# Performance work log

Hardware: AMD Instinct MI355X
Metric: run time of the kernel (lower is better)

## Reference

```python
import jax, jax.numpy as jnp
import numpy as np
from jax import lax

H, W = 32, 32
HEADS = 8
EPS_LN = 1e-5


def layer_norm(x, g, b):
    mu = jnp.mean(x, axis=-1, keepdims=True)
    var = jnp.mean((x - mu) ** 2, axis=-1, keepdims=True)
    return (x - mu) * lax.rsqrt(var + EPS_LN) * g + b


def l2norm(x):  # F.normalize along last dim, eps=1e-12
    n = jnp.sqrt(jnp.sum(x * x, axis=-1, keepdims=True))
    return x / jnp.maximum(n, 1e-12)


def channel_attention(x, qkv_w, temp, proj_w, proj_b):
    B, N, C = x.shape
    d = C // HEADS
    qkv = (x @ qkv_w).reshape(B, N, 3, HEADS, d).transpose(2, 0, 3, 1, 4)  # [3,B,h,N,d]
    q, k, v = qkv[0], qkv[1], qkv[2]
    q = l2norm(q.swapaxes(-2, -1))  # [B,h,d,N], normalized over N
    k = l2norm(k.swapaxes(-2, -1))
    v = v.swapaxes(-2, -1)          # [B,h,d,N]
    attn = jnp.einsum('bhdn,bhen->bhde', q, k) * temp  # [B,h,d,d]
    attn = jax.nn.softmax(attn, axis=-1)
    out = jnp.einsum('bhde,bhen->bhdn', attn, v)       # [B,h,d,N]
    out = out.transpose(0, 3, 1, 2).reshape(B, N, C)
    return out @ proj_w + proj_b


def cross_attention(x1, x2, rp_w, rp_b, cn_g, cn_b):
    # head_count = 1 (efficient/linear attention)
    B, N, D = x1.shape
    keys = x2.swapaxes(1, 2)            # [B,D,N]
    values = x1.swapaxes(1, 2)          # [B,D,N]
    key = jax.nn.softmax(keys, axis=2)  # softmax over tokens
    query = jax.nn.softmax(keys, axis=1)  # softmax over channels
    context = jnp.einsum('bdn,ben->bde', key, values)     # [B,Dk,Dv]
    attended = jnp.einsum('bde,bdn->ben', context, query)  # [B,Dv,N]
    agg = attended.reshape(B, D, H, W)
    # 1x1 conv reprojection D -> 2D
    rep = jnp.einsum('bdhw,ed->behw', agg, rp_w) + rp_b[None, :, None, None]
    rep = rep.reshape(B, 2 * D, N).transpose(0, 2, 1)     # [B,N,2D]
    return layer_norm(rep, cn_g, cn_b)


def mix_ffn(x, fc1_w, fc1_b, dw_w, dw_b, fc2_w, fc2_b):
    B, N, _ = x.shape
    c2 = fc1_w.shape[1]
    h1 = x @ fc1_w + fc1_b                                 # [B,N,c2]
    t = h1.swapaxes(1, 2).reshape(B, c2, H, W)
    conv = lax.conv_general_dilated(
        t, dw_w, window_strides=(1, 1), padding='SAME',
        feature_group_count=c2,
        dimension_numbers=('NCHW', 'OIHW', 'NCHW')) + dw_b[None, :, None, None]
    h2 = conv.reshape(B, c2, N).swapaxes(1, 2)             # [B,N,c2]
    return jax.nn.gelu(h2, approximate=False) @ fc2_w + fc2_b


def reference(x1, x2, ln1_g, ln1_b, ca_qkv_w, ca_temp, ca_proj_w, ca_proj_b,
              ln3_g, ln3_b, rp_w, rp_b, cn_g, cn_b, ln2_g, ln2_b,
              fc1_w, fc1_b, dw_w, dw_b, fc2_w, fc2_b):
    # NOTE: original code uses norm1 + channel_attn1 on BOTH streams
    channel1 = x1 + channel_attention(layer_norm(x1, ln1_g, ln1_b), ca_qkv_w, ca_temp, ca_proj_w, ca_proj_b)
    channel2 = x2 + channel_attention(layer_norm(x2, ln1_g, ln1_b), ca_qkv_w, ca_temp, ca_proj_w, ca_proj_b)
    n1 = layer_norm(channel1, ln3_g, ln3_b)
    n2 = layer_norm(channel2, ln3_g, ln3_b)
    attn = cross_attention(n1, n2, rp_w, rp_b, cn_g, cn_b)
    tx = jnp.concatenate([channel1, channel2], axis=2) + attn  # [B,N,2D]
    mx = tx + mix_ffn(layer_norm(tx, ln2_g, ln2_b), fc1_w, fc1_b, dw_w, dw_b, fc2_w, fc2_b)
    return mx


def setup_inputs() -> dict:
    key = jax.random.key(0)
    ks = jax.random.split(key, 8)
    B, N, D = 16, 1024, 384
    s = 0.02
    return {
        'x1': jax.random.normal(ks[0], (B, N, D), jnp.float32),
        'x2': jax.random.normal(ks[1], (B, N, D), jnp.float32),
        'ln1_g': jnp.ones((D,), jnp.float32), 'ln1_b': jnp.zeros((D,), jnp.float32),
        'ca_qkv_w': jax.random.normal(ks[2], (D, 3 * D), jnp.float32) * s,
        'ca_temp': jnp.ones((HEADS, 1, 1), jnp.float32),
        'ca_proj_w': jax.random.normal(ks[3], (D, D), jnp.float32) * s,
        'ca_proj_b': jnp.zeros((D,), jnp.float32),
        'ln3_g': jnp.ones((D,), jnp.float32), 'ln3_b': jnp.zeros((D,), jnp.float32),
        'rp_w': jax.random.normal(ks[4], (2 * D, D), jnp.float32) * s,
        'rp_b': jnp.zeros((2 * D,), jnp.float32),
        'cn_g': jnp.ones((2 * D,), jnp.float32), 'cn_b': jnp.zeros((2 * D,), jnp.float32),
        'ln2_g': jnp.ones((2 * D,), jnp.float32), 'ln2_b': jnp.zeros((2 * D,), jnp.float32),
        'fc1_w': jax.random.normal(ks[5], (2 * D, 4 * D), jnp.float32) * s,
        'fc1_b': jnp.zeros((4 * D,), jnp.float32),
        'dw_w': jax.random.normal(ks[6], (4 * D, 1, 3, 3), jnp.float32) * s,
        'dw_b': jnp.zeros((4 * D,), jnp.float32),
        'fc2_w': jax.random.normal(ks[7], (4 * D, 2 * D), jnp.float32) * s,
        'fc2_b': jnp.zeros((2 * D,), jnp.float32),
    }
```

## Files before the change

### kernel.cpp

```cpp
#include <hip/hip_runtime.h>
#include <math.h>

#define BN 16
#define NN 1024
#define DD 384
#define D2 768
#define C2 1536
#define NHEAD 8
#define DH 48

#define SZ_ND   (BN*NN*DD)
#define SZ_N2D  (BN*NN*D2)
#define SZ_NC2  (BN*NN*C2)
#define SZ_QKV  (BN*NN*3*DD)

typedef __bf16 bf16x8 __attribute__((ext_vector_type(8)));
typedef float f32x4v __attribute__((ext_vector_type(4)));
typedef unsigned short u16x4 __attribute__((ext_vector_type(4)));

__device__ __forceinline__ unsigned short f2bf(float x){
  unsigned int u = __float_as_uint(x);
  u += 0x7FFFu + ((u >> 16) & 1u);
  return (unsigned short)(u >> 16);
}
__device__ __forceinline__ float bf2f(unsigned short h){
  return __uint_as_float(((unsigned int)h) << 16);
}

__device__ __forceinline__ float blockReduceSum256(float v){
  __shared__ float red[4];
  #pragma unroll
  for (int o=32;o;o>>=1) v += __shfl_down(v,o,64);
  if ((threadIdx.x&63)==0) red[threadIdx.x>>6]=v;
  __syncthreads();
  float r = red[0]+red[1]+red[2]+red[3];
  __syncthreads();
  return r;
}
__device__ __forceinline__ float blockReduceMax256(float v){
  __shared__ float red[4];
  #pragma unroll
  for (int o=32;o;o>>=1) v = fmaxf(v, __shfl_down(v,o,64));
  if ((threadIdx.x&63)==0) red[threadIdx.x>>6]=v;
  __syncthreads();
  float r = fmaxf(fmaxf(red[0],red[1]),fmaxf(red[2],red[3]));
  __syncthreads();
  return r;
}

__global__ __launch_bounds__(256) void ln_kernel(const float* __restrict__ in,
    const float* __restrict__ g, const float* __restrict__ b,
    float* __restrict__ out, int C){
  const int row = blockIdx.x;
  const float* x = in + (size_t)row*C;
  float s=0.f;
  for (int i=threadIdx.x;i<C;i+=256) s += x[i];
  s = blockReduceSum256(s);
  const float mu = s / (float)C;
  float v=0.f;
  for (int i=threadIdx.x;i<C;i+=256){ float d = x[i]-mu; v += d*d; }
  v = blockReduceSum256(v);
  const float rs = rsqrtf(v/(float)C + 1e-5f);
  float* o = out + (size_t)row*C;
  for (int i=threadIdx.x;i<C;i+=256) o[i] = (x[i]-mu)*rs*g[i] + b[i];
}

__global__ __launch_bounds__(256) void ln_split_kernel(const float* __restrict__ in,
    const float* __restrict__ g, const float* __restrict__ b,
    unsigned short* __restrict__ oh, unsigned short* __restrict__ ol, int C){
  const int row = blockIdx.x;
  const float* x = in + (size_t)row*C;
  float s=0.f;
  for (int i=threadIdx.x;i<C;i+=256) s += x[i];
  s = blockReduceSum256(s);
  const float mu = s / (float)C;
  float v=0.f;
  for (int i=threadIdx.x;i<C;i+=256){ float d = x[i]-mu; v += d*d; }
  v = blockReduceSum256(v);
  const float rs = rsqrtf(v/(float)C + 1e-5f);
  unsigned short* ohp = oh + (size_t)row*C;
  unsigned short* olp = ol + (size_t)row*C;
  for (int i=threadIdx.x;i<C;i+=256){
    float val = (x[i]-mu)*rs*g[i] + b[i];
    unsigned short hh = f2bf(val);
    ohp[i] = hh; olp[i] = f2bf(val - bf2f(hh));
  }
}

__global__ __launch_bounds__(256) void rowsoftmax_split_kernel(const float* __restrict__ in,
    unsigned short* __restrict__ oh, unsigned short* __restrict__ ol, int C){
  const int row = blockIdx.x;
  const float* x = in + (size_t)row*C;
  float m = -3.0e38f;
  for (int i=threadIdx.x;i<C;i+=256) m = fmaxf(m, x[i]);
  m = blockReduceMax256(m);
  float s = 0.f;
  for (int i=threadIdx.x;i<C;i+=256) s += expf(x[i]-m);
  s = blockReduceSum256(s);
  const float inv = 1.f/s;
  unsigned short* ohp = oh + (size_t)row*C;
  unsigned short* olp = ol + (size_t)row*C;
  for (int i=threadIdx.x;i<C;i+=256){
    float p = expf(x[i]-m)*inv;
    unsigned short hh = f2bf(p);
    ohp[i] = hh; olp[i] = f2bf(p - bf2f(hh));
  }
}

__global__ __launch_bounds__(256) void colsoftmax_tsplit_kernel(const float* __restrict__ in,
    unsigned short* __restrict__ oh, unsigned short* __restrict__ ol){
  const int dl = threadIdx.x & 63;
  const int nc = threadIdx.x >> 6;
  const int d  = blockIdx.x*64 + dl;
  const int b  = blockIdx.y;
  const float* p = in + (size_t)b*NN*DD + d;
  __shared__ float redm[4][64];
  __shared__ float reds[4][64];
  float m = -3.0e38f;
  for (int n=nc*256; n<nc*256+256; n++) m = fmaxf(m, p[(size_t)n*DD]);
  redm[nc][dl] = m; __syncthreads();
  m = fmaxf(fmaxf(redm[0][dl],redm[1][dl]),fmaxf(redm[2][dl],redm[3][dl]));
  float s=0.f;
  for (int n=nc*256;n<nc*256+256;n++) s += expf(p[(size_t)n*DD]-m);
  reds[nc][dl]=s; __syncthreads();
  s = reds[0][dl]+reds[1][dl]+reds[2][dl]+reds[3][dl];
  const float inv = 1.f/s;
  unsigned short* qh = oh + ((size_t)b*DD + d)*NN;
  unsigned short* ql = ol + ((size_t)b*DD + d)*NN;
  for (int n=nc*256;n<nc*256+256;n++){
    float val = expf(p[(size_t)n*DD]-m)*inv;
    unsigned short hh = f2bf(val);
    qh[n] = hh; ql[n] = f2bf(val - bf2f(hh));
  }
}

__global__ __launch_bounds__(256) void tsplit_kernel(const float* __restrict__ in,
    unsigned short* __restrict__ oh, unsigned short* __restrict__ ol, int R, int Cc){
  const size_t zb = (size_t)blockIdx.z * R * Cc;
  const float* ip = in + zb;
  unsigned short* ohp = oh + zb;
  unsigned short* olp = ol + zb;
  __shared__ float tile[32][33];
  const int c0 = blockIdx.x*32, r0 = blockIdx.y*32;
  const int j = threadIdx.x & 31, i4 = threadIdx.x >> 5;
  #pragma unroll
  for (int s=0;s<4;s++){
    int i = i4*4+s;
    tile[i][j] = ip[(size_t)(r0+i)*Cc + c0 + j];
  }
  __syncthreads();
  #pragma unroll
  for (int s=0;s<4;s++){
    int i = i4*4+s;
    float x = tile[j][i];
    unsigned short h = f2bf(x);
    ohp[(size_t)(c0+i)*R + r0 + j] = h;
    olp[(size_t)(c0+i)*R + r0 + j] = f2bf(x - bf2f(h));
  }
}

__global__ __launch_bounds__(256) void chattn_mfma_kernel(
    const unsigned short* __restrict__ qh, const unsigned short* __restrict__ ql,
    const float* __restrict__ temp,
    unsigned short* __restrict__ coh, unsigned short* __restrict__ col)
{
  const int bh = blockIdx.x, b = bh >> 3, h = bh & 7;
  const int t = threadIdx.x, w = t >> 6, lane = t & 63;
  const int lr = lane & 15, g = lane >> 4;

  __shared__ __align__(16) unsigned char ldsA[27648];
  unsigned short (*Qh)[72] = (unsigned short(*)[72])(ldsA);
  unsigned short (*Ql)[72] = (unsigned short(*)[72])(ldsA + 6912);
  unsigned short (*Kh)[72] = (unsigned short(*)[72])(ldsA + 13824);
  unsigned short (*Kl)[72] = (unsigned short(*)[72])(ldsA + 20736);
  unsigned short (*Vh)[72] = (unsigned short(*)[72])(ldsA);
  unsigned short (*Vl)[72] = (unsigned short(*)[72])(ldsA + 9216);
  __shared__ unsigned short Ph[48][72], Pl[48][72];
  __shared__ float S[48][49];
  __shared__ float qn[48], kn[48];

  const size_t base = (size_t)b*NN*1152 + (size_t)h*48;

  int agrp[3], apr[3], aoff[3];
  #pragma unroll
  for (int l=0;l<3;l++){
    int idx = l*256+t;
    int mo = (idx>=384) ? 1 : 0;
    int a = idx - mo*384;
    agrp[l] = a%12; apr[l] = a/12; aoff[l] = mo*384;
  }

  f32x4v acc[12];
  #pragma unroll
  for (int i=0;i<12;i++) acc[i] = (f32x4v){0.f,0.f,0.f,0.f};

  u16x4 ch0[3], ch1_[3], cl0[3], cl1[3];
  #pragma unroll
  for (int l=0;l<3;l++){
    const size_t a = base + (size_t)(apr[l]*2)*1152 + aoff[l] + agrp[l]*4;
    ch0[l] = *(const u16x4*)(qh + a);
    ch1_[l]= *(const u16x4*)(qh + a + 1152);
    cl0[l] = *(const u16x4*)(ql + a);
    cl1[l] = *(const u16x4*)(ql + a + 1152);
  }

  for (int nc=0; nc<16; nc++){
    #pragma unroll
    for (int l=0;l<3;l++){
      unsigned short (*Dh)[72] = aoff[l] ? Kh : Qh;
      unsigned short (*Dl)[72] = aoff[l] ? Kl : Ql;
      #pragma unroll
      for (int c=0;c<4;c++){
        int d = agrp[l]*4+c;
        *(unsigned int*)&Dh[d][apr[l]*2] = (unsigned)ch0[l][c] | ((unsigned)ch1_[l][c]<<16);
        *(unsigned int*)&Dl[d][apr[l]*2] = (unsigned)cl0[l][c] | ((unsigned)cl1[l][c]<<16);
      }
    }
    __syncthreads();
    if (nc < 15){
      #pragma unroll
      for (int l=0;l<3;l++){
        const size_t a = base + (size_t)((nc+1)*64 + apr[l]*2)*1152 + aoff[l] + agrp[l]*4;
        ch0[l] = *(const u16x4*)(qh + a);
        ch1_[l]= *(const u16x4*)(qh + a + 1152);
        cl0[l] = *(const u16x4*)(ql + a);
        cl1[l] = *(const u16x4*)(ql + a + 1152);
      }
    }
    if (w < 3){
      #pragma unroll
      for (int ks=0;ks<2;ks++){
        bf16x8 a_h = *(const bf16x8*)&Qh[w*16+lr][ks*32+g*8];
        bf16x8 a_l = *(const bf16x8*)&Ql[w*16+lr][ks*32+g*8];
        #pragma unroll
        for (int c=0;c<3;c++){
          bf16x8 b_h = *(const bf16x8*)&Kh[c*16+lr][ks*32+g*8];
          bf16x8 b_l = *(const bf16x8*)&Kl[c*16+lr][ks*32+g*8];
          acc[c] = __builtin_amdgcn_mfma_f32_16x16x32_bf16(a_h, b_h, acc[c], 0,0,0);
          acc[c] = __builtin_amdgcn_mfma_f32_16x16x32_bf16(a_l, b_h, acc[c], 0,0,0);
          acc[c] = __builtin_amdgcn_mfma_f32_16x16x32_bf16(a_h, b_l, acc[c], 0,0,0);
        }
      }
    } else {
      #pragma unroll
      for (int ks=0;ks<2;ks++){
        #pragma unroll
        for (int c=0;c<3;c++){
          bf16x8 qh_ = *(const bf16x8*)&Qh[c*16+lr][ks*32+g*8];
          bf16x8 ql_ = *(const bf16x8*)&Ql[c*16+lr][ks*32+g*8];
          bf16x8 kh_ = *(const bf16x8*)&Kh[c*16+lr][ks*32+g*8];
          bf16x8 kl_ = *(const bf16x8*)&Kl[c*16+lr][ks*32+g*8];
          acc[c]   = __builtin_amdgcn_mfma_f32_16x16x32_bf16(qh_, qh_, acc[c],   0,0,0);
          acc[3+c] = __builtin_amdgcn_mfma_f32_16x16x32_bf16(qh_, ql_, acc[3+c], 0,0,0);
          acc[6+c] = __builtin_amdgcn_mfma_f32_16x16x32_bf16(kh_, kh_, acc[6+c], 0,0,0);
          acc[9+c] = __builtin_amdgcn_mfma_f32_16x16x32_bf16(kh_, kl_, acc[9+c], 0,0,0);
        }
      }
    }
    __syncthreads();
  }

  const float tp = temp[h];
  if (w == 3){
    if ((lane>>4) == ((lane&15)>>2)){
      int p = lane & 15, r = p & 3;
      #pragma unroll
      for (int c=0;c<3;c++){
        float q2 = fmaxf(acc[c][r]   + 2.f*acc[3+c][r], 0.f);
        float k2 = fmaxf(acc[6+c][r] + 2.f*acc[9+c][r], 0.f);
        qn[c*16+p] = fmaxf(sqrtf(q2), 1e-12f);
        kn[c*16+p] = fmaxf(sqrtf(k2), 1e-12f);
      }
    }
  }
  __syncthreads();
  if (w < 3){
    #pragma unroll
    for (int c=0;c<3;c++){
      #pragma unroll
      for (int r=0;r<4;r++){
        int i = w*16 + g*4 + r, j = c*16 + lr;
        S[i][j] = acc[c][r]*tp/(qn[i]*kn[j]);
      }
    }
  }
  __syncthreads();

  int vgrp[3], vtk[3];
  #pragma unroll
  for (int l=0;l<3;l++){ int idx=l*256+t; vtk[l]=idx/12; vgrp[l]=idx%12; }
  u16x4 pvh[3], pvl[3];
  #pragma unroll
  for (int l=0;l<3;l++){
    const size_t a = base + (size_t)vtk[l]*1152 + 768 + vgrp[l]*4;
    pvh[l] = *(const u16x4*)(qh + a);
    pvl[l] = *(const u16x4*)(ql + a);
  }

  if (t < 48){
    float m = -3.0e38f;
    for (int j=0;j<48;j++) m = fmaxf(m, S[t][j]);
    float s = 0.f;
    for (int j=0;j<48;j++){ float e_ = expf(S[t][j]-m); S[t][j] = e_; s += e_; }
    float inv = 1.f/s;
    for (int j=0;j<48;j++){
      float p = S[t][j]*inv;
      unsigned short hp = f2bf(p);
      Ph[t][j] = hp; Pl[t][j] = f2bf(p - bf2f(hp));
    }
    #pragma unroll
    for (int j=48;j<64;j++){ Ph[t][j]=0; Pl[t][j]=0; }
  } else {
    const u16x4 z4 = (u16x4){0,0,0,0};
    for (int idx=t-48; idx<512; idx+=208){
      int tk = idx>>3, q = idx&7;
      if (q<4) *(u16x4*)&Vh[tk][48+(q&3)*4] = z4;
      else     *(u16x4*)&Vl[tk][48+(q&3)*4] = z4;
    }
  }
  __syncthreads();

  bf16x8 pfh[3][2], pfl[3][2];
  #pragma unroll
  for (int it=0;it<3;it++)
    #pragma unroll
    for (int ks=0;ks<2;ks++){
      pfh[it][ks] = *(const bf16x8*)&Ph[it*16+lr][ks*32+g*8];
      pfl[it][ks] = *(const bf16x8*)&Pl[it*16+lr][ks*32+g*8];
    }

  for (int vc=0; vc<16; vc++){
    #pragma unroll
    for (int l=0;l<3;l++){
      *(u16x4*)&Vh[vtk[l]][vgrp[l]*4] = pvh[l];
      *(u16x4*)&Vl[vtk[l]][vgrp[l]*4] = pvl[l];
    }
    __syncthreads();
    if (vc < 15){
      #pragma unroll
      for (int l=0;l<3;l++){
        const size_t a = base + (size_t)((vc+1)*64+vtk[l])*1152 + 768 + vgrp[l]*4;
        pvh[l] = *(const u16x4*)(qh + a);
        pvl[l] = *(const u16x4*)(ql + a);
      }
    }
    bf16x8 vfh[2], vfl[2];
    #pragma unroll
    for (int ks=0;ks<2;ks++){
      vfh[ks] = *(const bf16x8*)&Vh[w*16+lr][ks*32+g*8];
      vfl[ks] = *(const bf16x8*)&Vl[w*16+lr][ks*32+g*8];
    }
    f32x4v o[3];
    #pragma unroll
    for (int it=0;it<3;it++) o[it] = (f32x4v){0.f,0.f,0.f,0.f};
    #pragma unroll
    for (int it=0;it<3;it++)
      #pragma unroll
      for (int ks=0;ks<2;ks++){
        o[it] = __builtin_amdgcn_mfma_f32_16x16x32_bf16(pfh[it][ks], vfh[ks], o[it], 0,0,0);
        o[it] = __builtin_amdgcn_mfma_f32_16x16x32_bf16(pfl[it][ks], vfh[ks], o[it], 0,0,0);
        o[it] = __builtin_amdgcn_mfma_f32_16x16x32_bf16(pfh[it][ks], vfl[ks], o[it], 0,0,0);
      }
    const int n = vc*64 + w*16 + lr;
    #pragma unroll
    for (int it=0;it<3;it++){
      const size_t off = ((size_t)b*NN + n)*DD + h*48 + it*16 + g*4;
      u16x4 hv, lv;
      #pragma unroll
      for (int r=0;r<4;r++){
        float x = o[it][r];
        unsigned short hh = f2bf(x);
        hv[r] = hh; lv[r] = f2bf(x - bf2f(hh));
      }
      *(u16x4*)(coh + off) = hv;
      *(u16x4*)(col + off) = lv;
    }
    __syncthreads();
  }
}

__global__ __launch_bounds__(256) void wconv_t_kernel(const float* __restrict__ in,
    unsigned short* __restrict__ oh, unsigned short* __restrict__ ol, int K, int Nin){
  __shared__ float tile[32][33];
  const int n0 = blockIdx.x*32, k0 = blockIdx.y*32;
  const int j = threadIdx.x & 31, i4 = threadIdx.x >> 5;
  #pragma unroll
  for (int s=0;s<4;s++){
    int i = i4*4+s;
    tile[i][j] = (n0 + j < Nin) ? in[(size_t)(k0+i)*Nin + n0 + j] : 0.f;
  }
  __syncthreads();
  #pragma unroll
  for (int s=0;s<4;s++){
    int i = i4*4+s;
    float x = tile[j][i];
    unsigned short h = f2bf(x);
    oh[(size_t)(n0+i)*K + k0 + j] = h;
    ol[(size_t)(n0+i)*K + k0 + j] = f2bf(x - bf2f(h));
  }
}

__global__ __launch_bounds__(256) void wconv_kernel(const float* __restrict__ in,
    unsigned short* __restrict__ oh, unsigned short* __restrict__ ol, int n){
  int i = blockIdx.x*256 + threadIdx.x;
  if (i < n){
    float x = in[i];
    unsigned short h = f2bf(x);
    oh[i] = h;
    ol[i] = f2bf(x - bf2f(h));
  }
}

template<bool BIAS_, bool RES_, bool SPLIT_>
__global__ __launch_bounds__(256) void gemm_bf16x3s_kernel(
    const unsigned short* __restrict__ Ah, const unsigned short* __restrict__ Al,
    const unsigned short* __restrict__ Bh, const unsigned short* __restrict__ Bl,
    const float* __restrict__ bias, const float* __restrict__ res,
    float* __restrict__ C, unsigned short* __restrict__ Ch, unsigned short* __restrict__ Cl,
    int M, int N, int K, size_t sAz, size_t sBz, size_t sCz)
{
  const int t = threadIdx.x;
  const int nwg = gridDim.x*gridDim.y;
  const int lin = blockIdx.y*gridDim.x + blockIdx.x;
  const int swz = ((nwg & 7)==0) ? ((lin & 7)*(nwg >> 3) + (lin >> 3)) : lin;
  const int bx = swz % gridDim.x, by = swz / gridDim.x;
  const int m0 = by*128, n0 = bx*128;
  const size_t zo = (size_t)blockIdx.z;

  __shared__ unsigned short As_h0[128][32], As_l0[128][32];
  __shared__ unsigned short Bs_h0[128][32], Bs_l0[128][32];
  __shared__ unsigned short As_h1[128][32], As_l1[128][32];
  __shared__ unsigned short Bs_h1[128][32], Bs_l1[128][32];

  const unsigned short* Ahb = Ah + zo*sAz + (size_t)m0*K;
  const unsigned short* Alb = Al + zo*sAz + (size_t)m0*K;
  const unsigned short* Bhb = Bh + zo*sBz + (size_t)n0*K;
  const unsigned short* Blb = Bl + zo*sBz + (size_t)n0*K;

  f32x4v acc[4][4];
  #pragma unroll
  for (int i=0;i<4;i++)
    #pragma unroll
    for (int j=0;j<4;j++) acc[i][j] = (f32x4v){0.f,0.f,0.f,0.f};

  const int w  = t >> 6;
  const int wm = w >> 1, wn = w & 1;
  const int lr = t & 15, g = (t & 63) >> 4;
  const int srow = t >> 1;
  const int kb0  = (t & 1)*2;
  const int ssw  = (srow >> 1) & 3;
  const int ks0  = ((kb0+0) ^ ssw)*8;
  const int ks1  = ((kb0+1) ^ ssw)*8;

  uint4 aAh0,aAh1,aAl0,aAl1,aBh0,aBh1,aBl0,aBl1;
  uint4 bAh0,bAh1,bAl0,bAl1,bBh0,bBh1,bBl0,bBl1;

#define LOADT(P, K0) { \
    const size_t go0 = (size_t)srow*K + (size_t)(K0) + (size_t)(kb0*8); \
    P##Ah0 = *(const uint4*)(Ahb + go0); P##Ah1 = *(const uint4*)(Ahb + go0 + 8); \
    P##Al0 = *(const uint4*)(Alb + go0); P##Al1 = *(const uint4*)(Alb + go0 + 8); \
    P##Bh0 = *(const uint4*)(Bhb + go0); P##Bh1 = *(const uint4*)(Bhb + go0 + 8); \
    P##Bl0 = *(const uint4*)(Blb + go0); P##Bl1 = *(const uint4*)(Blb + go0 + 8); }

#define WRITET(BUF, P) { \
    *(uint4*)&As_h##BUF[srow][ks0] = P##Ah0; *(uint4*)&As_h##BUF[srow][ks1] = P##Ah1; \
    *(uint4*)&As_l##BUF[srow][ks0] = P##Al0; *(uint4*)&As_l##BUF[srow][ks1] = P##Al1; \
    *(uint4*)&Bs_h##BUF[srow][ks0] = P##Bh0; *(uint4*)&Bs_h##BUF[srow][ks1] = P##Bh1; \
    *(uint4*)&Bs_l##BUF[srow][ks0] = P##Bl0; *(uint4*)&Bs_l##BUF[srow][ks1] = P##Bl1; }

#define COMPUTET(BUF) { \
    bf16x8 ah[4], al[4], bhf[4], blf[4]; \
    _Pragma("unroll") \
    for (int i=0;i<4;i++){ \
      const int ra = wm*64 + i*16 + lr; \
      const int ka = (g ^ ((ra>>1)&3))*8; \
      ah[i]  = *(const bf16x8*)&As_h##BUF[ra][ka]; \
      al[i]  = *(const bf16x8*)&As_l##BUF[ra][ka]; \
      const int rb = wn*64 + i*16 + lr; \
      const int kb = (g ^ ((rb>>1)&3))*8; \
      bhf[i] = *(const bf16x8*)&Bs_h##BUF[rb][kb]; \
      blf[i] = *(const bf16x8*)&Bs_l##BUF[rb][kb]; \
    } \
    _Pragma("unroll") \
    for (int mi=0;mi<4;mi++) \
      _Pragma("unroll") \
      for (int ni=0;ni<4;ni++){ \
        f32x4v c_ = acc[mi][ni]; \
        c_ = __builtin_amdgcn_mfma_f32_16x16x32_bf16(ah[mi], bhf[ni], c_, 0,0,0); \
        c_ = __builtin_amdgcn_mfma_f32_16x16x32_bf16(al[mi], bhf[ni], c_, 0,0,0); \
        c_ = __builtin_amdgcn_mfma_f32_16x16x32_bf16(ah[mi], blf[ni], c_, 0,0,0); \
        acc[mi][ni] = c_; \
      } }

  const int nk = K >> 5;
  LOADT(a, 0);
  WRITET(0, a);
  LOADT(a, 32);
  __syncthreads();

  for (int kt = 0; kt < nk; kt += 2){
    if (kt+2 < nk) LOADT(b, (kt+2)*32);
    COMPUTET(0);
    WRITET(1, a);
    __syncthreads();
    if (kt+3 < nk) LOADT(a, (kt+3)*32);
    COMPUTET(1);
    if (kt+2 < nk){ WRITET(0, b); }
    __syncthreads();
  }

#undef LOADT
#undef WRITET
#undef COMPUTET

  if (SPLIT_){
    unsigned short* Chb = Ch + zo*sCz;
    unsigned short* Clb = Cl + zo*sCz;
    #pragma unroll
    for (int ni=0;ni<4;ni++){
      const int col = n0 + wn*64 + ni*16 + lr;
      #pragma unroll
      for (int mi=0;mi<4;mi++){
        const int r0 = m0 + wm*64 + mi*16 + g*4;
        #pragma unroll
        for (int r=0;r<4;r++){
          float v = acc[mi][ni][r];
          unsigned short hv = f2bf(v);
          const size_t off = (size_t)(r0+r)*N + col;
          Chb[off] = hv;
          Clb[off] = f2bf(v - bf2f(hv));
        }
      }
    }
  } else {
    float* Cb = C + zo*sCz;
    const float* resb = RES_ ? (res + zo*sCz) : nullptr;
    #pragma unroll
    for (int ni=0;ni<4;ni++){
      const int col = n0 + wn*64 + ni*16 + lr;
      const float bb = BIAS_ ? bias[col] : 0.f;
      #pragma unroll
      for (int mi=0;mi<4;mi++){
        const int r0 = m0 + wm*64 + mi*16 + g*4;
        #pragma unroll
        for (int r=0;r<4;r++){
          float v = acc[mi][ni][r] + bb;
          if (RES_) v += resb[(size_t)(r0+r)*N + col];
          Cb[(size_t)(r0+r)*N + col] = v;
        }
      }
    }
  }
}

__global__ __launch_bounds__(256) void ln_concat_ln2_kernel(const float* __restrict__ rep,
    const float* __restrict__ g1, const float* __restrict__ b1,
    const float* __restrict__ ch1, const float* __restrict__ ch2,
    const float* __restrict__ g2, const float* __restrict__ b2,
    float* __restrict__ tx, unsigned short* __restrict__ y2h, unsigned short* __restrict__ y2l){
  const int row = blockIdx.x;
  const float* x = rep + (size_t)row*D2;
  float xv[3];
  float s=0.f;
  #pragma unroll
  for (int q=0;q<3;q++){ xv[q] = x[threadIdx.x + q*256]; s += xv[q]; }
  s = blockReduceSum256(s);
  const float mu = s / (float)D2;
  float v=0.f;
  #pragma unroll
  for (int q=0;q<3;q++){ float d = xv[q]-mu; v += d*d; }
  v = blockReduceSum256(v);
  const float rs = rsqrtf(v/(float)D2 + 1e-5f);
  float tv[3];
  #pragma unroll
  for (int q=0;q<3;q++){
    int i = threadIdx.x + q*256;
    float val = (xv[q]-mu)*rs*g1[i] + b1[i];
    float rv = (i<DD) ? ch1[(size_t)row*DD + i] : ch2[(size_t)row*DD + i - DD];
    tv[q] = val + rv;
    tx[(size_t)row*D2 + i] = tv[q];
  }
  float s2 = tv[0]+tv[1]+tv[2];
  s2 = blockReduceSum256(s2);
  const float mu2 = s2 / (float)D2;
  float v2=0.f;
  #pragma unroll
  for (int q=0;q<3;q++){ float d = tv[q]-mu2; v2 += d*d; }
  v2 = blockReduceSum256(v2);
  const float rs2 = rsqrtf(v2/(float)D2 + 1e-5f);
  #pragma unroll
  for (int q=0;q<3;q++){
    int i = threadIdx.x + q*256;
    float y = (tv[q]-mu2)*rs2*g2[i] + b2[i];
    unsigned short hh = f2bf(y);
    y2h[(size_t)row*D2 + i] = hh;
    y2l[(size_t)row*D2 + i] = f2bf(y - bf2f(hh));
  }
}

__global__ __launch_bounds__(256) void dwconv_gelu_kernel(const float* __restrict__ h1,
    const float* __restrict__ w, const float* __restrict__ bias,
    unsigned short* __restrict__ gh, unsigned short* __restrict__ gl){
  const int idx = blockIdx.x*256 + threadIdx.x;
  const int b   = idx / 12288;
  const int r   = idx - b*12288;
  const int hh  = r / 384;
  const int c4  = r - hh*384;
  const int c   = c4*4;
  const float* base = h1 + (size_t)b*NN*C2 + c;
  const size_t obase = ((size_t)b*NN + hh*32)*C2 + c;

  f32x4v wk[9];
  #pragma unroll
  for (int k=0;k<9;k++){
    f32x4v t_;
    #pragma unroll
    for (int q=0;q<4;q++) t_[q] = w[(size_t)(c+q)*9 + k];
    wk[k] = t_;
  }
  f32x4v bvv;
  {
    const float4 bb = *(const float4*)(bias + c);
    bvv = (f32x4v){bb.x, bb.y, bb.z, bb.w};
  }

  const bool hm = (hh > 0), hp = (hh < 31);
  const f32x4v z4 = (f32x4v){0.f,0.f,0.f,0.f};
  const size_t rm = (size_t)((hh-1)*32)*C2;
  const size_t r0 = (size_t)( hh   *32)*C2;
  const size_t rp = (size_t)((hh+1)*32)*C2;

  f32x4v A0,A1,A2, B0,B1,B2, C0,C1,C2c;
  A0=z4; A1=z4; A2=z4;
  B0 = hm ? *(const f32x4v*)(base + rm) : z4;
  B1 =      *(const f32x4v*)(base + r0);
  B2 = hp ? *(const f32x4v*)(base + rp) : z4;
  C0 = hm ? *(const f32x4v*)(base + rm + C2) : z4;
  C1 =      *(const f32x4v*)(base + r0 + C2);
  C2c= hp ? *(const f32x4v*)(base + rp + C2) : z4;

  for (int ww=0; ww<32; ww++){
    f32x4v N0,N1,N2;
    if (ww < 30){
      const size_t co_ = (size_t)(ww+2)*C2;
      N0 = hm ? *(const f32x4v*)(base + rm + co_) : z4;
      N1 =      *(const f32x4v*)(base + r0 + co_) ;
      N2 = hp ? *(const f32x4v*)(base + rp + co_) : z4;
    } else { N0=z4; N1=z4; N2=z4; }

    f32x4v s = bvv;
    s += wk[0]*A0 + wk[1]*B0 + wk[2]*C0;
    s += wk[3]*A1 + wk[4]*B1 + wk[5]*C1;
    s += wk[6]*A2 + wk[7]*B2 + wk[8]*C2c;

    u16x4 hv, lv;
    #pragma unroll
    for (int q=0;q<4;q++){
      float rlt = 0.5f*s[q]*(1.f + erff(s[q]*0.70710678118654752f));
      unsigned short hhv = f2bf(rlt);
      hv[q] = hhv; lv[q] = f2bf(rlt - bf2f(hhv));
    }
    *(u16x4*)(gh + obase + (size_t)ww*C2) = hv;
    *(u16x4*)(gl + obase + (size_t)ww*C2) = lv;

    A0=B0; A1=B1; A2=B2;
    B0=C0; B1=C1; B2=C2c;
    C0=N0; C1=N1; C2c=N2;
  }
}

extern "C" void kernel_launch(void* const* d_in, const int* in_sizes, int n_in,
                              void* d_out, int out_size, void* d_ws, size_t ws_size,
                              hipStream_t stream) {
  const float* x1     = (const float*)d_in[0];
  const float* x2     = (const float*)d_in[1];
  const float* ln1_g  = (const float*)d_in[2];
  const float* ln1_b  = (const float*)d_in[3];
  const float* qkv_w  = (const float*)d_in[4];
  const float* ca_temp= (const float*)d_in[5];
  const float* proj_w = (const float*)d_in[6];
  const float* proj_b = (const float*)d_in[7];
  const float* ln3_g  = (const float*)d_in[8];
  const float* ln3_b  = (const float*)d_in[9];
  const float* rp_w   = (const float*)d_in[10];
  const float* rp_b   = (const float*)d_in[11];
  const float* cn_g   = (const float*)d_in[12];
  const float* cn_b   = (const float*)d_in[13];
  const float* ln2_g  = (const float*)d_in[14];
  const float* ln2_b  = (const float*)d_in[15];
  const float* fc1_w  = (const float*)d_in[16];
  const float* fc1_b  = (const float*)d_in[17];
  const float* dw_w   = (const float*)d_in[18];
  const float* dw_b   = (const float*)d_in[19];
  const float* fc2_w  = (const float*)d_in[20];
  const float* fc2_b  = (const float*)d_in[21];
  float* out = (float*)d_out;
  float* W   = (float*)d_ws;

  unsigned short* ycoh = (unsigned short*)W;
  unsigned short* ycol = ycoh + (size_t)SZ_ND;
  unsigned short* coh  = ycoh;
  unsigned short* col  = ycol;
  unsigned short* qkvh = (unsigned short*)(W + (size_t)SZ_ND);
  unsigned short* qkvl = qkvh + (size_t)SZ_QKV;
  float* ch1  = W + 25165824ull;
  float* ch2  = W + 31457280ull;
  unsigned short* qkvwT_h  = (unsigned short*)(W + 37748736ull);
  unsigned short* qkvwT_l  = qkvwT_h + 442368u;
  unsigned short* projwT_h = qkvwT_l + 442368u;
  unsigned short* projwT_l = projwT_h + 147456u;
  float* n1  = W;
  float* n2  = W + (size_t)SZ_ND;
  unsigned short* KSt_h = (unsigned short*)(W + 2ull*SZ_ND);
  unsigned short* KSt_l = KSt_h + (size_t)SZ_ND;
  unsigned short* QSh = (unsigned short*)(W + 3ull*SZ_ND);
  unsigned short* QSl = QSh + (size_t)SZ_ND;
  unsigned short* rpw_h = (unsigned short*)(W + 37748736ull);
  unsigned short* rpw_l = rpw_h + 294912u;
  unsigned short* n1t_h = (unsigned short*)(W + 38043648ull);
  unsigned short* n1t_l = n1t_h + (size_t)SZ_ND;
  unsigned short* ctxT_h = (unsigned short*)W;
  unsigned short* ctxT_l = ctxT_h + 2359296u;
  unsigned short* ATbh = (unsigned short*)(W + 2ull*SZ_ND);
  unsigned short* ATbl = ATbh + (size_t)SZ_ND;
  float* rep = W;
  float* txp  = out;
  float* h1   = W;
  unsigned short* y2h = (unsigned short*)(W + 25165824ull);
  unsigned short* y2l = y2h + (size_t)SZ_N2D;
  unsigned short* fc1wT_h = (unsigned short*)(W + 37748736ull);
  unsigned short* fc1wT_l = fc1wT_h + 1179648u;
  unsigned short* gh = (unsigned short*)(W + 25165824ull);
  unsigned short* gl = gh + (size_t)SZ_NC2;
  unsigned short* fc2wT_h = (unsigned short*)W;
  unsigned short* fc2wT_l = fc2wT_h + 1179648u;

  const int M = BN*NN;

  wconv_t_kernel<<<dim3(1152/32, DD/32), dim3(256), 0, stream>>>(qkv_w, qkvwT_h, qkvwT_l, DD, 1152);
  wconv_t_kernel<<<dim3(DD/32, DD/32), dim3(256), 0, stream>>>(proj_w, projwT_h, projwT_l, DD, DD);

  ln_split_kernel<<<dim3(M), dim3(256), 0, stream>>>(x1, ln1_g, ln1_b, ycoh, ycol, DD);
  gemm_bf16x3s_kernel<false,false,true><<<dim3(1152/128, M/128), dim3(256), 0, stream>>>(
      ycoh, ycol, qkvwT_h, qkvwT_l, nullptr, nullptr, nullptr, qkvh, qkvl, M, 1152, DD, 0,0,0);
  chattn_mfma_kernel<<<dim3(BN*NHEAD), dim3(256), 0, stream>>>(qkvh, qkvl, ca_temp, coh, col);
  gemm_bf16x3s_kernel<true,true,false><<<dim3(DD/128, M/128), dim3(256), 0, stream>>>(
      coh, col, projwT_h, projwT_l, proj_b, x1, ch1, nullptr, nullptr, M, DD, DD, 0,0,0);

  ln_split_kernel<<<dim3(M), dim3(256), 0, stream>>>(x2, ln1_g, ln1_b, ycoh, ycol, DD);
  gemm_bf16x3s_kernel<false,false,true><<<dim3(1152/128, M/128), dim3(256), 0, stream>>>(
      ycoh, ycol, qkvwT_h, qkvwT_l, nullptr, nullptr, nullptr, qkvh, qkvl, M, 1152, DD, 0,0,0);
  chattn_mfma_kernel<<<dim3(BN*NHEAD), dim3(256), 0, stream>>>(qkvh, qkvl, ca_temp, coh, col);
  gemm_bf16x3s_kernel<true,true,false><<<dim3(DD/128, M/128), dim3(256), 0, stream>>>(
      coh, col, projwT_h, projwT_l, proj_b, x2, ch2, nullptr, nullptr, M, DD, DD, 0,0,0);

  wconv_kernel<<<dim3(294912/256), dim3(256), 0, stream>>>(rp_w, rpw_h, rpw_l, 294912);
  ln_kernel<<<dim3(M), dim3(256), 0, stream>>>(ch1, ln3_g, ln3_b, n1, DD);
  ln_kernel<<<dim3(M), dim3(256), 0, stream>>>(ch2, ln3_g, ln3_b, n2, DD);
  rowsoftmax_split_kernel<<<dim3(M), dim3(256), 0, stream>>>(n2, QSh, QSl, DD);
  colsoftmax_tsplit_kernel<<<dim3(DD/64, BN), dim3(256), 0, stream>>>(n2, KSt_h, KSt_l);
  tsplit_kernel<<<dim3(DD/32, NN/32, BN), dim3(256), 0, stream>>>(n1, n1t_h, n1t_l, NN, DD);
  gemm_bf16x3s_kernel<false,false,true><<<dim3(DD/128, DD/128, BN), dim3(256), 0, stream>>>(
      n1t_h, n1t_l, KSt_h, KSt_l, nullptr, nullptr, nullptr, ctxT_h, ctxT_l,
      DD, DD, NN, (size_t)DD*NN, (size_t)DD*NN, (size_t)DD*DD);
  gemm_bf16x3s_kernel<false,false,true><<<dim3(DD/128, NN/128, BN), dim3(256), 0, stream>>>(
      QSh, QSl, ctxT_h, ctxT_l, nullptr, nullptr, nullptr, ATbh, ATbl,
      NN, DD, DD, (size_t)NN*DD, (size_t)DD*DD, (size_t)NN*DD);
  gemm_bf16x3s_kernel<true,false,false><<<dim3(D2/128, M/128), dim3(256), 0, stream>>>(
      ATbh, ATbl, rpw_h, rpw_l, rp_b, nullptr, rep, nullptr, nullptr, M, D2, DD, 0,0,0);
  ln_concat_ln2_kernel<<<dim3(M), dim3(256), 0, stream>>>(
      rep, cn_g, cn_b, ch1, ch2, ln2_g, ln2_b, txp, y2h, y2l);

  wconv_t_kernel<<<dim3(C2/32, D2/32), dim3(256), 0, stream>>>(fc1_w, fc1wT_h, fc1wT_l, D2, C2);
  gemm_bf16x3s_kernel<true,false,false><<<dim3(C2/128, M/128), dim3(256), 0, stream>>>(
      y2h, y2l, fc1wT_h, fc1wT_l, fc1_b, nullptr, h1, nullptr, nullptr, M, C2, D2, 0,0,0);
  dwconv_gelu_kernel<<<dim3(196608/256), dim3(256), 0, stream>>>(h1, dw_w, dw_b, gh, gl);
  wconv_t_kernel<<<dim3(D2/32, C2/32), dim3(256), 0, stream>>>(fc2_w, fc2wT_h, fc2wT_l, C2, D2);
  gemm_bf16x3s_kernel<true,true,false><<<dim3(D2/128, M/128), dim3(256), 0, stream>>>(
      gh, gl, fc2wT_h, fc2wT_l, fc2_b, txp, out, nullptr, nullptr, M, D2, C2, 0,0,0);
}
```

Measured before the change: 975.9 us.

## Batch the x1 and x2 channel-attention branches into single double-height launches

Runs the LN1, QKV GEMM, channel attention and projection GEMM for x1 and x2 as one launch each over 32768 rows instead of two sequential launches over 16384 rows. The residual epilogue picks x1 or x2 by row block, and LN3 runs once over both halves. This halves the launch count and doubles the grid of the small proj GEMM (3x128 tiles) to fill the GPU better. The workspace is reorganized to fit the larger QKV buffers, and the output buffer is borrowed as scratch, so the aliasing must stay correct.

```diff
diff --git a/kernel.cpp b/kernel.cpp
--- a/kernel.cpp
+++ b/kernel.cpp
@@ -12,7 +12,8 @@
 #define SZ_ND   (BN*NN*DD)
 #define SZ_N2D  (BN*NN*D2)
 #define SZ_NC2  (BN*NN*C2)
-#define SZ_QKV  (BN*NN*3*DD)
+#define M2      32768
+#define MH      16384
 
 typedef __bf16 bf16x8 __attribute__((ext_vector_type(8)));
 typedef float f32x4v __attribute__((ext_vector_type(4)));
@@ -65,11 +66,12 @@
   for (int i=threadIdx.x;i<C;i+=256) o[i] = (x[i]-mu)*rs*g[i] + b[i];
 }
 
-__global__ __launch_bounds__(256) void ln_split_kernel(const float* __restrict__ in,
+__global__ __launch_bounds__(256) void ln_split2_kernel(const float* __restrict__ in1,
+    const float* __restrict__ in2, int Mh,
     const float* __restrict__ g, const float* __restrict__ b,
     unsigned short* __restrict__ oh, unsigned short* __restrict__ ol, int C){
   const int row = blockIdx.x;
-  const float* x = in + (size_t)row*C;
+  const float* x = (row < Mh) ? (in1 + (size_t)row*C) : (in2 + (size_t)(row-Mh)*C);
   float s=0.f;
   for (int i=threadIdx.x;i<C;i+=256) s += x[i];
   s = blockReduceSum256(s);
@@ -416,6 +418,7 @@
     const unsigned short* __restrict__ Ah, const unsigned short* __restrict__ Al,
     const unsigned short* __restrict__ Bh, const unsigned short* __restrict__ Bl,
     const float* __restrict__ bias, const float* __restrict__ res,
+    const float* __restrict__ res2, int Mh2,
     float* __restrict__ C, unsigned short* __restrict__ Ch, unsigned short* __restrict__ Cl,
     int M, int N, int K, size_t sAz, size_t sBz, size_t sCz)
 {
@@ -534,7 +537,12 @@
     }
   } else {
     float* Cb = C + zo*sCz;
-    const float* resb = RES_ ? (res + zo*sCz) : nullptr;
+    const float* resb = nullptr;
+    size_t roff = 0;
+    if (RES_){
+      if (res2 != nullptr && m0 >= Mh2){ resb = res2; roff = (size_t)Mh2; }
+      else resb = res + zo*sCz;
+    }
     #pragma unroll
     for (int ni=0;ni<4;ni++){
       const int col = n0 + wn*64 + ni*16 + lr;
@@ -545,7 +553,7 @@
         #pragma unroll
         for (int r=0;r<4;r++){
           float v = acc[mi][ni][r] + bb;
-          if (RES_) v += resb[(size_t)(r0+r)*N + col];
+          if (RES_) v += resb[((size_t)(r0+r) - roff)*N + col];
           Cb[(size_t)(r0+r)*N + col] = v;
         }
       }
@@ -697,85 +705,79 @@
   float* out = (float*)d_out;
   float* W   = (float*)d_ws;
 
-  unsigned short* ycoh = (unsigned short*)W;
-  unsigned short* ycol = ycoh + (size_t)SZ_ND;
+  unsigned short* ycoh = (unsigned short*)out;
+  unsigned short* ycol = ycoh + 12582912u;
   unsigned short* coh  = ycoh;
   unsigned short* col  = ycol;
-  unsigned short* qkvh = (unsigned short*)(W + (size_t)SZ_ND);
-  unsigned short* qkvl = qkvh + (size_t)SZ_QKV;
-  float* ch1  = W + 25165824ull;
-  float* ch2  = W + 31457280ull;
+  unsigned short* qkvh = (unsigned short*)W;
+  unsigned short* qkvl = qkvh + 37748736u;
   unsigned short* qkvwT_h  = (unsigned short*)(W + 37748736ull);
   unsigned short* qkvwT_l  = qkvwT_h + 442368u;
   unsigned short* projwT_h = qkvwT_l + 442368u;
   unsigned short* projwT_l = projwT_h + 147456u;
-  float* n1  = W;
-  float* n2  = W + (size_t)SZ_ND;
-  unsigned short* KSt_h = (unsigned short*)(W + 2ull*SZ_ND);
-  unsigned short* KSt_l = KSt_h + (size_t)SZ_ND;
-  unsigned short* QSh = (unsigned short*)(W + 3ull*SZ_ND);
-  unsigned short* QSl = QSh + (size_t)SZ_ND;
+  float* ch12 = W;
+  float* n12  = W + 12582912ull;
+  unsigned short* QSh = (unsigned short*)(W + 25165824ull);
+  unsigned short* QSl = QSh + 6291456u;
+  unsigned short* KSt_h = (unsigned short*)(W + 31457280ull);
+  unsigned short* KSt_l = KSt_h + 6291456u;
   unsigned short* rpw_h = (unsigned short*)(W + 37748736ull);
   unsigned short* rpw_l = rpw_h + 294912u;
   unsigned short* n1t_h = (unsigned short*)(W + 38043648ull);
-  unsigned short* n1t_l = n1t_h + (size_t)SZ_ND;
-  unsigned short* ctxT_h = (unsigned short*)W;
+  unsigned short* n1t_l = n1t_h + 6291456u;
+  unsigned short* ctxT_h = (unsigned short*)(W + 12582912ull);
   unsigned short* ctxT_l = ctxT_h + 2359296u;
-  unsigned short* ATbh = (unsigned short*)(W + 2ull*SZ_ND);
-  unsigned short* ATbl = ATbh + (size_t)SZ_ND;
-  float* rep = W;
-  float* txp  = out;
-  float* h1   = W;
-  unsigned short* y2h = (unsigned short*)(W + 25165824ull);
-  unsigned short* y2l = y2h + (size_t)SZ_N2D;
-  unsigned short* fc1wT_h = (unsigned short*)(W + 37748736ull);
+  unsigned short* ATbh = (unsigned short*)(W + 14942208ull);
+  unsigned short* ATbl = ATbh + 6291456u;
+  float* rep = W + 25165824ull;
+  float* txp = out;
+  unsigned short* y2h = (unsigned short*)(W + 37748736ull);
+  unsigned short* y2l = y2h + 12582912u;
+  float* h1 = W;
+  unsigned short* fc1wT_h = (unsigned short*)(W + 25165824ull);
   unsigned short* fc1wT_l = fc1wT_h + 1179648u;
   unsigned short* gh = (unsigned short*)(W + 25165824ull);
-  unsigned short* gl = gh + (size_t)SZ_NC2;
+  unsigned short* gl = (unsigned short*)(W + 37748736ull);
   unsigned short* fc2wT_h = (unsigned short*)W;
   unsigned short* fc2wT_l = fc2wT_h + 1179648u;
 
-  const int M = BN*NN;
-
   wconv_t_kernel<<<dim3(1152/32, DD/32), dim3(256), 0, stream>>>(qkv_w, qkvwT_h, qkvwT_l, DD, 1152);
   wconv_t_kernel<<<dim3(DD/32, DD/32), dim3(256), 0, stream>>>(proj_w, projwT_h, projwT_l, DD, DD);
 
-  ln_split_kernel<<<dim3(M), dim3(256), 0, stream>>>(x1, ln1_g, ln1_b, ycoh, ycol, DD);
-  gemm_bf16x3s_kernel<false,false,true><<<dim3(1152/128, M/128), dim3(256), 0, stream>>>(
-      ycoh, ycol, qkvwT_h, qkvwT_l, nullptr, nullptr, nullptr, qkvh, qkvl, M, 1152, DD, 0,0,0);
-  chattn_mfma_kernel<<<dim3(BN*NHEAD), dim3(256), 0, stream>>>(qkvh, qkvl, ca_temp, coh, col);
-  gemm_bf16x3s_kernel<true,true,false><<<dim3(DD/128, M/128), dim3(256), 0, stream>>>(
-      coh, col, projwT_h, projwT_l, proj_b, x1, ch1, nullptr, nullptr, M, DD, DD, 0,0,0);
-
-  ln_split_kernel<<<dim3(M), dim3(256), 0, stream>>>(x2, ln1_g, ln1_b, ycoh, ycol, DD);
-  gemm_bf16x3s_kernel<false,false,true><<<dim3(1152/128, M/128), dim3(256), 0, stream>>>(
-      ycoh, ycol, qkvwT_h, qkvwT_l, nullptr, nullptr, nullptr, qkvh, qkvl, M, 1152, DD, 0,0,0);
-  chattn_mfma_kernel<<<dim3(BN*NHEAD), dim3(256), 0, stream>>>(qkvh, qkvl, ca_temp, coh, col);
-  gemm_bf16x3s_kernel<true,true,false><<<dim3(DD/128, M/128), dim3(256), 0, stream>>>(
-      coh, col, projwT_h, projwT_l, proj_b, x2, ch2, nullptr, nullptr, M, DD, DD, 0,0,0);
+  ln_split2_kernel<<<dim3(M2), dim3(256), 0, stream>>>(x1, x2, MH, ln1_g, ln1_b, ycoh, ycol, DD);
+  gemm_bf16x3s_kernel<false,false,true><<<dim3(1152/128, M2/128), dim3(256), 0, stream>>>(
+      ycoh, ycol, qkvwT_h, qkvwT_l, nullptr, nullptr, nullptr, 0,
+      nullptr, qkvh, qkvl, M2, 1152, DD, 0,0,0);
+  chattn_mfma_kernel<<<dim3(32*NHEAD), dim3(256), 0, stream>>>(qkvh, qkvl, ca_temp, coh, col);
+  gemm_bf16x3s_kernel<true,true,false><<<dim3(DD/128, M2/128), dim3(256), 0, stream>>>(
+      coh, col, projwT_h, projwT_l, proj_b, x1, x2, MH,
+      ch12, nullptr, nullptr, M2, DD, DD, 0,0,0);
 
   wconv_kernel<<<dim3(294912/256), dim3(256), 0, stream>>>(rp_w, rpw_h, rpw_l, 294912);
-  ln_kernel<<<dim3(M), dim3(256), 0, stream>>>(ch1, ln3_g, ln3_b, n1, DD);
-  ln_kernel<<<dim3(M), dim3(256), 0, stream>>>(ch2, ln3_g, ln3_b, n2, DD);
-  rowsoftmax_split_kernel<<<dim3(M), dim3(256), 0, stream>>>(n2, QSh, QSl, DD);
-  colsoftmax_tsplit_kernel<<<dim3(DD/64, BN), dim3(256), 0, stream>>>(n2, KSt_h, KSt_l);
-  tsplit_kernel<<<dim3(DD/32, NN/32, BN), dim3(256), 0, stream>>>(n1, n1t_h, n1t_l, NN, DD);
+  ln_kernel<<<dim3(M2), dim3(256), 0, stream>>>(ch12, ln3_g, ln3_b, n12, DD);
+  const float* n2half = n12 + (size_t)MH*DD;
+  rowsoftmax_split_kernel<<<dim3(MH), dim3(256), 0, stream>>>(n2half, QSh, QSl, DD);
+  colsoftmax_tsplit_kernel<<<dim3(DD/64, BN), dim3(256), 0, stream>>>(n2half, KSt_h, KSt_l);
+  tsplit_kernel<<<dim3(DD/32, NN/32, BN), dim3(256), 0, stream>>>(n12, n1t_h, n1t_l, NN, DD);
   gemm_bf16x3s_kernel<false,false,true><<<dim3(DD/128, DD/128, BN), dim3(256), 0, stream>>>(
-      n1t_h, n1t_l, KSt_h, KSt_l, nullptr, nullptr, nullptr, ctxT_h, ctxT_l,
-      DD, DD, NN, (size_t)DD*NN, (size_t)DD*NN, (size_t)DD*DD);
+      n1t_h, n1t_l, KSt_h, KSt_l, nullptr, nullptr, nullptr, 0,
+      nullptr, ctxT_h, ctxT_l, DD, DD, NN, (size_t)DD*NN, (size_t)DD*NN, (size_t)DD*DD);
   gemm_bf16x3s_kernel<false,false,true><<<dim3(DD/128, NN/128, BN), dim3(256), 0, stream>>>(
-      QSh, QSl, ctxT_h, ctxT_l, nullptr, nullptr, nullptr, ATbh, ATbl,
-      NN, DD, DD, (size_t)NN*DD, (size_t)DD*DD, (size_t)NN*DD);
-  gemm_bf16x3s_kernel<true,false,false><<<dim3(D2/128, M/128), dim3(256), 0, stream>>>(
-      ATbh, ATbl, rpw_h, rpw_l, rp_b, nullptr, rep, nullptr, nullptr, M, D2, DD, 0,0,0);
-  ln_concat_ln2_kernel<<<dim3(M), dim3(256), 0, stream>>>(
-      rep, cn_g, cn_b, ch1, ch2, ln2_g, ln2_b, txp, y2h, y2l);
+      QSh, QSl, ctxT_h, ctxT_l, nullptr, nullptr, nullptr, 0,
+      nullptr, ATbh, ATbl, NN, DD, DD, (size_t)NN*DD, (size_t)DD*DD, (size_t)NN*DD);
+  gemm_bf16x3s_kernel<true,false,false><<<dim3(D2/128, MH/128), dim3(256), 0, stream>>>(
+      ATbh, ATbl, rpw_h, rpw_l, rp_b, nullptr, nullptr, 0,
+      rep, nullptr, nullptr, MH, D2, DD, 0,0,0);
+  ln_concat_ln2_kernel<<<dim3(MH), dim3(256), 0, stream>>>(
+      rep, cn_g, cn_b, ch12, ch12 + (size_t)MH*DD, ln2_g, ln2_b, txp, y2h, y2l);
 
   wconv_t_kernel<<<dim3(C2/32, D2/32), dim3(256), 0, stream>>>(fc1_w, fc1wT_h, fc1wT_l, D2, C2);
-  gemm_bf16x3s_kernel<true,false,false><<<dim3(C2/128, M/128), dim3(256), 0, stream>>>(
-      y2h, y2l, fc1wT_h, fc1wT_l, fc1_b, nullptr, h1, nullptr, nullptr, M, C2, D2, 0,0,0);
+  gemm_bf16x3s_kernel<true,false,false><<<dim3(C2/128, MH/128), dim3(256), 0, stream>>>(
+      y2h, y2l, fc1wT_h, fc1wT_l, fc1_b, nullptr, nullptr, 0,
+      h1, nullptr, nullptr, MH, C2, D2, 0,0,0);
   dwconv_gelu_kernel<<<dim3(196608/256), dim3(256), 0, stream>>>(h1, dw_w, dw_b, gh, gl);
   wconv_t_kernel<<<dim3(D2/32, C2/32), dim3(256), 0, stream>>>(fc2_w, fc2wT_h, fc2wT_l, C2, D2);
-  gemm_bf16x3s_kernel<true,true,false><<<dim3(D2/128, M/128), dim3(256), 0, stream>>>(
-      gh, gl, fc2wT_h, fc2wT_l, fc2_b, txp, out, nullptr, nullptr, M, D2, C2, 0,0,0);
-}
+  gemm_bf16x3s_kernel<true,true,false><<<dim3(D2/128, MH/128), dim3(256), 0, stream>>>(
+      gh, gl, fc2wT_h, fc2wT_l, fc2_b, txp, nullptr, 0,
+      out, nullptr, nullptr, MH, D2, C2, 0,0,0);
+}
```

Result: faster. 918.7 us (-5.9%).
